# Kernel optimization log

Hardware: AMD Instinct MI355X
Metric: run time of the kernel (lower is better)

## Reference

```python
import jax, jax.numpy as jnp
from jax import lax
import numpy as np

H = 256

def _cell(x, h, c, wih, whh, bih, bhh):
    # PyTorch LSTMCell: gates ordered i, f, g, o
    g = x @ wih.T + bih + h @ whh.T + bhh
    i, f, gg, o = jnp.split(g, 4, axis=-1)
    c = jax.nn.sigmoid(f) * c + jax.nn.sigmoid(i) * jnp.tanh(gg)
    h = jax.nn.sigmoid(o) * jnp.tanh(c)
    return h, c


def setup_inputs() -> dict:
    key = jax.random.key(0)
    ks = iter(jax.random.split(key, 64))
    def lin(out_f, in_f):
        s = 1.0 / np.sqrt(in_f)
        w = jax.random.uniform(next(ks), (out_f, in_f), minval=-s, maxval=s, dtype=jnp.float32)
        b = jax.random.uniform(next(ks), (out_f,), minval=-s, maxval=s, dtype=jnp.float32)
        return w, b
    def cellp():
        s = 1.0 / np.sqrt(H)
        return tuple(jax.random.uniform(next(ks), sh, minval=-s, maxval=s, dtype=jnp.float32)
                     for sh in [(4 * H, H), (4 * H, H), (4 * H,), (4 * H,)])
    d = {}
    d['x'] = jax.random.normal(next(ks), (20, 256, 64, 64), dtype=jnp.float32)
    d['fc_en1_w'], d['fc_en1_b'] = lin(1024, 4096)
    d['fc_en2_w'], d['fc_en2_b'] = lin(H, 1024)
    for nm in ['en1', 'en2', 'en3', 'de1', 'de2', 'de3']:
        d[nm + '_wih'], d[nm + '_whh'], d[nm + '_bih'], d[nm + '_bhh'] = cellp()
    d['fc_de1_w'], d['fc_de1_b'] = lin(1024, H)
    d['fc_de2_w'], d['fc_de2_b'] = lin(4096, 1024)
    d['future_step'] = 10
    return d


def reference(x, fc_en1_w, fc_en1_b, fc_en2_w, fc_en2_b,
              en1_wih, en1_whh, en1_bih, en1_bhh,
              en2_wih, en2_whh, en2_bih, en2_bhh,
              en3_wih, en3_whh, en3_bih, en3_bhh,
              de1_wih, de1_whh, de1_bih, de1_bhh,
              de2_wih, de2_whh, de2_bih, de2_bhh,
              de3_wih, de3_whh, de3_bih, de3_bhh,
              fc_de1_w, fc_de1_b, fc_de2_w, fc_de2_b, future_step):
    seq, B = x.shape[0], x.shape[1]
    xf = x.reshape(seq, B, -1)  # (S, B, 4096)
    z0 = jnp.zeros((B, H), x.dtype)

    def enc_step(carry, xt):
        h1, c1, h2, c2, h3, c3 = carry
        z = jax.nn.relu(xt @ fc_en1_w.T + fc_en1_b)
        z = jax.nn.relu(z @ fc_en2_w.T + fc_en2_b)
        h1, c1 = _cell(z, h1, c1, en1_wih, en1_whh, en1_bih, en1_bhh)
        h2, c2 = _cell(h1, h2, c2, en2_wih, en2_whh, en2_bih, en2_bhh)
        h3, c3 = _cell(h2, h3, c3, en3_wih, en3_whh, en3_bih, en3_bhh)
        return (h1, c1, h2, c2, h3, c3), None

    enc_carry, _ = lax.scan(enc_step, (z0,) * 6, xf)
    h_e3 = enc_carry[4]

    def dec_step(carry, _):
        h1, c1, h2, c2, h3, c3 = carry
        h1, c1 = _cell(z0, h1, c1, de1_wih, de1_whh, de1_bih, de1_bhh)
        h2, c2 = _cell(h1, h2, c2, de2_wih, de2_whh, de2_bih, de2_bhh)
        h3, c3 = _cell(h2, h3, c3, de3_wih, de3_whh, de3_bih, de3_bhh)
        y = jax.nn.relu(h3 @ fc_de1_w.T + fc_de1_b)
        y = jnp.tanh(y @ fc_de2_w.T + fc_de2_b)
        return (h1, c1, h2, c2, h3, c3), y

    _, ys = lax.scan(dec_step, (h_e3, z0, z0, z0, z0, z0), None, length=future_step)
    return ys.reshape(future_step, B, 64, 64)
```

## Files before the change

### kernel.cpp

```cpp
#include <hip/hip_runtime.h>
#include <math.h>

static __device__ __forceinline__ float sigf(float v) { return 1.0f / (1.0f + expf(-v)); }

using s8v = __attribute__((ext_vector_type(8))) short;
using f4v = __attribute__((ext_vector_type(4))) float;

static __device__ __forceinline__ void splitf(float f, unsigned short& h, unsigned short& l) {
  unsigned u = __float_as_uint(f);
  unsigned short hb = (unsigned short)((u + 0x7FFFu + ((u >> 16) & 1u)) >> 16);
  float hf = __uint_as_float(((unsigned)hb) << 16);
  float lf = f - hf;
  unsigned ul = __float_as_uint(lf);
  unsigned short lb = (unsigned short)((ul + 0x7FFFu + ((ul >> 16) & 1u)) >> 16);
  h = hb; l = lb;
}

__global__ __launch_bounds__(256) void wsplit(
    const float* __restrict__ W, unsigned short* __restrict__ WH,
    unsigned short* __restrict__ WL, int n4)
{
  int i = blockIdx.x * 256 + threadIdx.x;
  if (i < n4) {
    float4 v = ((const float4*)W)[i];
    ushort4 h, l;
    splitf(v.x, h.x, l.x); splitf(v.y, h.y, l.y);
    splitf(v.z, h.z, l.z); splitf(v.w, h.w, l.w);
    ((ushort4*)WH)[i] = h;
    ((ushort4*)WL)[i] = l;
  }
}

template <int OSPLIT>
__global__ __launch_bounds__(256) void gemm_sf(
    const float* __restrict__ A,
    const unsigned short* __restrict__ WH, const unsigned short* __restrict__ WL,
    const float* __restrict__ bias, float* __restrict__ C,
    unsigned short* __restrict__ OH, unsigned short* __restrict__ OL,
    int M, int N, int K, int act)
{
  __shared__ unsigned short AsH[128 * 40];
  __shared__ unsigned short AsL[128 * 40];
  __shared__ unsigned short WsH[64 * 40];
  __shared__ unsigned short WsL[64 * 40];

  const int t = threadIdx.x;
  const int w = t >> 6, lane = t & 63;
  const int lrow = lane & 15, lk = (lane >> 4) * 8;
  const int m0 = blockIdx.x * 128, n0 = blockIdx.y * 64;

  f4v acc[2][4];
#pragma unroll
  for (int i = 0; i < 2; ++i)
#pragma unroll
    for (int j = 0; j < 4; ++j) acc[i][j] = (f4v){0.f, 0.f, 0.f, 0.f};

  for (int k0 = 0; k0 < K; k0 += 32) {
#pragma unroll
    for (int i = 0; i < 4; ++i) {
      int v = i * 256 + t;
      int row = v >> 3, kq = (v & 7) << 2;
      float4 a = *(const float4*)(A + (size_t)(m0 + row) * K + k0 + kq);
      ushort4 h4, l4;
      splitf(a.x, h4.x, l4.x); splitf(a.y, h4.y, l4.y);
      splitf(a.z, h4.z, l4.z); splitf(a.w, h4.w, l4.w);
      *(ushort4*)&AsH[row * 40 + kq] = h4;
      *(ushort4*)&AsL[row * 40 + kq] = l4;
    }
    {
      int row = t >> 2, q = (t & 3) * 8;
      *(s8v*)&WsH[row * 40 + q] = *(const s8v*)(WH + (size_t)(n0 + row) * K + k0 + q);
      *(s8v*)&WsL[row * 40 + q] = *(const s8v*)(WL + (size_t)(n0 + row) * K + k0 + q);
    }
    __syncthreads();

    s8v aH[2], aL[2], bH[4], bL[4];
#pragma unroll
    for (int mt = 0; mt < 2; ++mt) {
      int r = (w * 32 + mt * 16 + lrow) * 40 + lk;
      aH[mt] = *(const s8v*)&AsH[r];
      aL[mt] = *(const s8v*)&AsL[r];
    }
#pragma unroll
    for (int nt = 0; nt < 4; ++nt) {
      int r = (nt * 16 + lrow) * 40 + lk;
      bH[nt] = *(const s8v*)&WsH[r];
      bL[nt] = *(const s8v*)&WsL[r];
    }
#pragma unroll
    for (int mt = 0; mt < 2; ++mt)
#pragma unroll
      for (int nt = 0; nt < 4; ++nt) {
        acc[mt][nt] = __builtin_amdgcn_mfma_f32_16x16x32_bf16(aH[mt], bH[nt], acc[mt][nt], 0, 0, 0);
        acc[mt][nt] = __builtin_amdgcn_mfma_f32_16x16x32_bf16(aH[mt], bL[nt], acc[mt][nt], 0, 0, 0);
        acc[mt][nt] = __builtin_amdgcn_mfma_f32_16x16x32_bf16(aL[mt], bH[nt], acc[mt][nt], 0, 0, 0);
      }
    __syncthreads();
  }

#pragma unroll
  for (int mt = 0; mt < 2; ++mt)
#pragma unroll
    for (int nt = 0; nt < 4; ++nt) {
      int gcol = n0 + nt * 16 + lrow;
      float bv = bias[gcol];
#pragma unroll
      for (int r = 0; r < 4; ++r) {
        int grow = m0 + w * 32 + mt * 16 + (lane >> 4) * 4 + r;
        float v = acc[mt][nt][r] + bv;
        if (act == 1) v = fmaxf(v, 0.f);
        else if (act == 2) v = tanhf(v);
        if (OSPLIT) {
          unsigned short h, l;
          splitf(v, h, l);
          OH[(size_t)grow * N + gcol] = h;
          OL[(size_t)grow * N + gcol] = l;
        } else {
          C[(size_t)grow * N + gcol] = v;
        }
      }
    }
}

template <int OSPLIT>
__global__ __launch_bounds__(256) void gemm_bb(
    const unsigned short* __restrict__ AH, const unsigned short* __restrict__ AL,
    const unsigned short* __restrict__ WH, const unsigned short* __restrict__ WL,
    const float* __restrict__ bias, float* __restrict__ C,
    unsigned short* __restrict__ OH, unsigned short* __restrict__ OL,
    int M, int N, int K, int act)
{
  __shared__ unsigned short AsH[128 * 40];
  __shared__ unsigned short AsL[128 * 40];
  __shared__ unsigned short WsH[64 * 40];
  __shared__ unsigned short WsL[64 * 40];

  const int t = threadIdx.x;
  const int w = t >> 6, lane = t & 63;
  const int lrow = lane & 15, lk = (lane >> 4) * 8;
  const int m0 = blockIdx.x * 128, n0 = blockIdx.y * 64;

  f4v acc[2][4];
#pragma unroll
  for (int i = 0; i < 2; ++i)
#pragma unroll
    for (int j = 0; j < 4; ++j) acc[i][j] = (f4v){0.f, 0.f, 0.f, 0.f};

  for (int k0 = 0; k0 < K; k0 += 32) {
#pragma unroll
    for (int i = 0; i < 2; ++i) {
      int v = i * 256 + t;
      int row = v >> 2, q = (v & 3) * 8;
      *(s8v*)&AsH[row * 40 + q] = *(const s8v*)(AH + (size_t)(m0 + row) * K + k0 + q);
      *(s8v*)&AsL[row * 40 + q] = *(const s8v*)(AL + (size_t)(m0 + row) * K + k0 + q);
    }
    {
      int row = t >> 2, q = (t & 3) * 8;
      *(s8v*)&WsH[row * 40 + q] = *(const s8v*)(WH + (size_t)(n0 + row) * K + k0 + q);
      *(s8v*)&WsL[row * 40 + q] = *(const s8v*)(WL + (size_t)(n0 + row) * K + k0 + q);
    }
    __syncthreads();

    s8v aH[2], aL[2], bH[4], bL[4];
#pragma unroll
    for (int mt = 0; mt < 2; ++mt) {
      int r = (w * 32 + mt * 16 + lrow) * 40 + lk;
      aH[mt] = *(const s8v*)&AsH[r];
      aL[mt] = *(const s8v*)&AsL[r];
    }
#pragma unroll
    for (int nt = 0; nt < 4; ++nt) {
      int r = (nt * 16 + lrow) * 40 + lk;
      bH[nt] = *(const s8v*)&WsH[r];
      bL[nt] = *(const s8v*)&WsL[r];
    }
#pragma unroll
    for (int mt = 0; mt < 2; ++mt)
#pragma unroll
      for (int nt = 0; nt < 4; ++nt) {
        acc[mt][nt] = __builtin_amdgcn_mfma_f32_16x16x32_bf16(aH[mt], bH[nt], acc[mt][nt], 0, 0, 0);
        acc[mt][nt] = __builtin_amdgcn_mfma_f32_16x16x32_bf16(aH[mt], bL[nt], acc[mt][nt], 0, 0, 0);
        acc[mt][nt] = __builtin_amdgcn_mfma_f32_16x16x32_bf16(aL[mt], bH[nt], acc[mt][nt], 0, 0, 0);
      }
    __syncthreads();
  }

#pragma unroll
  for (int mt = 0; mt < 2; ++mt)
#pragma unroll
    for (int nt = 0; nt < 4; ++nt) {
      int gcol = n0 + nt * 16 + lrow;
      float bv = bias[gcol];
#pragma unroll
      for (int r = 0; r < 4; ++r) {
        int grow = m0 + w * 32 + mt * 16 + (lane >> 4) * 4 + r;
        float v = acc[mt][nt][r] + bv;
        if (act == 1) v = fmaxf(v, 0.f);
        else if (act == 2) v = tanhf(v);
        if (OSPLIT) {
          unsigned short h, l;
          splitf(v, h, l);
          OH[(size_t)grow * N + gcol] = h;
          OL[(size_t)grow * N + gcol] = l;
        } else {
          C[(size_t)grow * N + gcol] = v;
        }
      }
    }
}

__global__ __launch_bounds__(256) void prep_pack(
    const float* __restrict__ wih, const float* __restrict__ whh,
    const float* __restrict__ bih, const float* __restrict__ bhh,
    float* __restrict__ wihP, float* __restrict__ whhP, float* __restrict__ bP)
{
  const int j = blockIdx.x, k = threadIdx.x;
  float4 a, c;
  a.x = wih[(0 * 256 + j) * 256 + k];
  a.y = wih[(1 * 256 + j) * 256 + k];
  a.z = wih[(2 * 256 + j) * 256 + k];
  a.w = wih[(3 * 256 + j) * 256 + k];
  *(float4*)&wihP[((size_t)j * 256 + k) * 4] = a;
  c.x = whh[(0 * 256 + j) * 256 + k];
  c.y = whh[(1 * 256 + j) * 256 + k];
  c.z = whh[(2 * 256 + j) * 256 + k];
  c.w = whh[(3 * 256 + j) * 256 + k];
  *(float4*)&whhP[((size_t)j * 256 + k) * 4] = c;
  if (k < 4) bP[j * 4 + k] = bih[k * 256 + j] + bhh[k * 256 + j];
}

__global__ __launch_bounds__(256) void transpose256(
    const float* __restrict__ in, float* __restrict__ out)
{
  const int t = blockIdx.x, c4 = blockIdx.y;
  const int r = threadIdx.x;
  float4 v = *(const float4*)(in + ((size_t)t * 256 + r) * 256 + c4 * 4);
  float* op = out + (size_t)t * 65536 + (size_t)(c4 * 4) * 256 + r;
  op[0]   = v.x;
  op[256] = v.y;
  op[512] = v.z;
  op[768] = v.w;
}

__global__ __launch_bounds__(256) void transpose256s(
    const float* __restrict__ in, unsigned short* __restrict__ outH,
    unsigned short* __restrict__ outL)
{
  const int t = blockIdx.x, c4 = blockIdx.y;
  const int r = threadIdx.x;
  float4 v = *(const float4*)(in + ((size_t)t * 256 + r) * 256 + c4 * 4);
  ushort4 h, l;
  splitf(v.x, h.x, l.x); splitf(v.y, h.y, l.y);
  splitf(v.z, h.z, l.z); splitf(v.w, h.w, l.w);
  size_t o = (size_t)t * 65536 + (size_t)(c4 * 4) * 256 + r;
  outH[o] = h.x; outH[o + 256] = h.y; outH[o + 512] = h.z; outH[o + 768] = h.w;
  outL[o] = l.x; outL[o + 256] = l.y; outL[o + 512] = l.z; outL[o + 768] = l.w;
}

struct CellSlot {
  const float* x;
  const float* wih;
  const float* whh;
  const float* bias;
  const float* hin;
  float* c;
  float* hout;
  float* hcopy;
  int hasx;
};
struct CellArgs { CellSlot s[3]; };

__global__ __launch_bounds__(512) void cell_multi(CellArgs args)
{
  __shared__ float part[4][64][4];
  const CellSlot S = args.s[blockIdx.x >> 8];
  const int inner = blockIdx.x & 255;
  const int jg = inner & 63, bg = inner >> 6;
  const int t = threadIdx.x;
  const int lane = t & 63;
  const int wave = t >> 6;
  const int jwv = wave & 3;
  const int kh = __builtin_amdgcn_readfirstlane(wave >> 2);
  const int b = bg * 64 + lane;

  const int jw = __builtin_amdgcn_readfirstlane(jg * 4 + jwv);
  const float4* wh = (const float4*)(S.whh + (size_t)jw * 1024) + kh * 128;
  const float4* wi = (const float4*)(S.wih + (size_t)jw * 1024) + kh * 128;
  const float* hcol = S.hin + (size_t)kh * 128 * 256 + b;

  float4 acc;
  if (kh == 0) acc = *(const float4*)(S.bias + jw * 4);
  else         acc = (float4){0.f, 0.f, 0.f, 0.f};

  if (S.hasx) {
    const float* xcol = S.x + (size_t)kh * 128 * 256 + b;
#pragma unroll 8
    for (int k = 0; k < 128; ++k) {
      const float hv = hcol[k * 256];
      const float4 wv = wh[k];
      acc.x = fmaf(hv, wv.x, acc.x);
      acc.y = fmaf(hv, wv.y, acc.y);
      acc.z = fmaf(hv, wv.z, acc.z);
      acc.w = fmaf(hv, wv.w, acc.w);
      const float xv = xcol[k * 256];
      const float4 vv = wi[k];
      acc.x = fmaf(xv, vv.x, acc.x);
      acc.y = fmaf(xv, vv.y, acc.y);
      acc.z = fmaf(xv, vv.z, acc.z);
      acc.w = fmaf(xv, vv.w, acc.w);
    }
  } else {
#pragma unroll 8
    for (int k = 0; k < 128; ++k) {
      const float hv = hcol[k * 256];
      const float4 wv = wh[k];
      acc.x = fmaf(hv, wv.x, acc.x);
      acc.y = fmaf(hv, wv.y, acc.y);
      acc.z = fmaf(hv, wv.z, acc.z);
      acc.w = fmaf(hv, wv.w, acc.w);
    }
  }

  if (kh == 1) *(float4*)&part[jwv][lane][0] = acc;
  __syncthreads();
  if (kh == 0) {
    const float4 p = *(const float4*)&part[jwv][lane][0];
    acc.x += p.x; acc.y += p.y; acc.z += p.z; acc.w += p.w;

    const int idx = jw * 256 + b;
    const float cold = S.c[idx];
    const float ig = sigf(acc.x), fg = sigf(acc.y);
    const float gg = tanhf(acc.z), og = sigf(acc.w);
    const float cn = fg * cold + ig * gg;
    const float hn = og * tanhf(cn);
    S.c[idx] = cn;
    S.hout[idx] = hn;
    if (S.hcopy) S.hcopy[idx] = hn;
  }
}


extern "C" void kernel_launch(void* const* d_in, const int* in_sizes, int n_in,
                              void* d_out, int out_size, void* d_ws, size_t ws_size,
                              hipStream_t stream)
{
  const float* x_in  = (const float*)d_in[0];
  const float* w_en1 = (const float*)d_in[1];
  const float* b_en1 = (const float*)d_in[2];
  const float* w_en2 = (const float*)d_in[3];
  const float* b_en2 = (const float*)d_in[4];
  const float* cw[6][4];
  for (int i = 0; i < 6; ++i)
    for (int j = 0; j < 4; ++j) cw[i][j] = (const float*)d_in[5 + i * 4 + j];
  const float* w_de1 = (const float*)d_in[29];
  const float* b_de1 = (const float*)d_in[30];
  const float* w_de2 = (const float*)d_in[31];
  const float* b_de2 = (const float*)d_in[32];
  float* out = (float*)d_out;

  float* fs   = (float*)d_ws;
  float* wihP = fs;
  float* whhP = wihP + 6 * 262144;
  float* bP   = whhP + 6 * 262144;
  float* hb   = bP + 6 * 1024;
  float* cb   = hb + 12 * 65536;
  float* H3T  = cb + 6 * 65536;
  float* z2   = H3T + 10 * 65536;
  float* z2T  = z2 + 1310720;
  unsigned short* us = (unsigned short*)(z2T + 1310720);
  unsigned short* WEN1H = us;              us += 4194304;
  unsigned short* WEN1L = us;              us += 4194304;
  unsigned short* WEN2H = us;              us += 262144;
  unsigned short* WEN2L = us;              us += 262144;
  unsigned short* WDE1H = us;              us += 262144;
  unsigned short* WDE1L = us;              us += 262144;
  unsigned short* WDE2H = us;              us += 4194304;
  unsigned short* WDE2L = us;              us += 4194304;
  unsigned short* Z1H   = us;              us += 5242880;
  unsigned short* Z1L   = us;              us += 5242880;
  unsigned short* H3H = Z1H;
  unsigned short* H3L = Z1H + 655360;
  unsigned short* Y1H = Z1H + 1310720;
  unsigned short* Y1L = Z1H + 1310720 + 2621440;

  for (int i = 0; i < 6; ++i)
    prep_pack<<<256, 256, 0, stream>>>(cw[i][0], cw[i][1], cw[i][2], cw[i][3],
                                       wihP + i * 262144, whhP + i * 262144,
                                       bP + i * 1024);
  wsplit<<<4096, 256, 0, stream>>>(w_en1, WEN1H, WEN1L, 1048576);
  wsplit<<<256, 256, 0, stream>>>(w_en2, WEN2H, WEN2L, 65536);
  wsplit<<<256, 256, 0, stream>>>(w_de1, WDE1H, WDE1L, 65536);
  wsplit<<<4096, 256, 0, stream>>>(w_de2, WDE2H, WDE2L, 1048576);
  hipMemsetAsync(hb, 0, (size_t)18 * 65536 * sizeof(float), stream);

  gemm_sf<1><<<dim3(40, 16), 256, 0, stream>>>(
      x_in, WEN1H, WEN1L, b_en1, nullptr, Z1H, Z1L, 5120, 1024, 4096, 1);
  gemm_bb<0><<<dim3(40, 4), 256, 0, stream>>>(
      Z1H, Z1L, WEN2H, WEN2L, b_en2, z2, nullptr, nullptr, 5120, 256, 1024, 1);
  transpose256<<<dim3(20, 64), 256, 0, stream>>>(z2, z2T);

  int pp[6] = {0, 0, 0, 0, 0, 0};
  auto HBuf = [&](int l, int p) { return hb + (size_t)(l * 2 + p) * 65536; };
  auto CBuf = [&](int l) { return cb + (size_t)l * 65536; };
  auto WI = [&](int l) { return wihP + (size_t)l * 262144; };
  auto WHp = [&](int l) { return whhP + (size_t)l * 262144; };
  auto BB = [&](int l) { return bP + (size_t)l * 1024; };

  for (int s = 0; s <= 21; ++s) {
    CellArgs a; int n = 0; int tog[3]; int nt = 0;
    if (s < 20) {
      a.s[n++] = {z2T + (size_t)s * 65536, WI(0), WHp(0), BB(0),
                  HBuf(0, pp[0]), CBuf(0), HBuf(0, pp[0] ^ 1), nullptr, 1};
      tog[nt++] = 0;
    }
    if (s >= 1 && s <= 20) {
      a.s[n++] = {HBuf(0, pp[0]), WI(1), WHp(1), BB(1),
                  HBuf(1, pp[1]), CBuf(1), HBuf(1, pp[1] ^ 1), nullptr, 1};
      tog[nt++] = 1;
    }
    if (s >= 2) {
      a.s[n++] = {HBuf(1, pp[1]), WI(2), WHp(2), BB(2),
                  HBuf(2, pp[2]), CBuf(2), HBuf(2, pp[2] ^ 1), nullptr, 1};
      tog[nt++] = 2;
    }
    cell_multi<<<n * 256, 512, 0, stream>>>(a);
    for (int i = 0; i < nt; ++i) pp[tog[i]] ^= 1;
  }

  for (int s = 0; s <= 11; ++s) {
    CellArgs a; int n = 0; int tog[3]; int nt = 0;
    if (s < 10) {
      const float* h1in = (s == 0) ? HBuf(2, pp[2]) : HBuf(3, pp[3]);
      a.s[n++] = {nullptr, WI(3), WHp(3), BB(3),
                  h1in, CBuf(3), HBuf(3, pp[3] ^ 1), nullptr, 0};
      tog[nt++] = 3;
    }
    if (s >= 1 && s <= 10) {
      a.s[n++] = {HBuf(3, pp[3]), WI(4), WHp(4), BB(4),
                  HBuf(4, pp[4]), CBuf(4), HBuf(4, pp[4] ^ 1), nullptr, 1};
      tog[nt++] = 4;
    }
    if (s >= 2) {
      a.s[n++] = {HBuf(4, pp[4]), WI(5), WHp(5), BB(5),
                  HBuf(5, pp[5]), CBuf(5), HBuf(5, pp[5] ^ 1),
                  H3T + (size_t)(s - 2) * 65536, 1};
      tog[nt++] = 5;
    }
    cell_multi<<<n * 256, 512, 0, stream>>>(a);
    for (int i = 0; i < nt; ++i) pp[tog[i]] ^= 1;
  }

  transpose256s<<<dim3(10, 64), 256, 0, stream>>>(H3T, H3H, H3L);
  gemm_bb<1><<<dim3(20, 16), 256, 0, stream>>>(
      H3H, H3L, WDE1H, WDE1L, b_de1, nullptr, Y1H, Y1L, 2560, 1024, 256, 1);
  gemm_bb<0><<<dim3(20, 64), 256, 0, stream>>>(
      Y1H, Y1L, WDE2H, WDE2L, b_de2, out, nullptr, nullptr, 2560, 4096, 1024, 2);

  (void)in_sizes; (void)n_in; (void)out_size; (void)ws_size;
}
```

Measured before the change: 874.9 us.

## Split LSTM cell reduction four ways and pre-split input for bf16x3 GEMM

The LSTM cell kernel now uses 1024 threads per block, splitting the K reduction into four 64-wide quarters instead of two halves. Partial sums are combined through shared memory, which shortens each thread's serial FMA chain in the latency-bound recurrent steps at the cost of more waves per block and extra reductions. Separately, when the workspace is large enough, the input x is pre-split into bf16 high/low halves and the first encoder GEMM uses the bf16-pair kernel instead of the float-input split-on-the-fly kernel. This adds a large extra pass over the 20M-element input and 80MB of workspace.

Result: slower. 903.2 us (+3.2%).

```diff
diff --git a/kernel.cpp b/kernel.cpp
--- a/kernel.cpp
+++ b/kernel.cpp
@@ -270,9 +270,9 @@
 };
 struct CellArgs { CellSlot s[3]; };
 
-__global__ __launch_bounds__(512) void cell_multi(CellArgs args)
-{
-  __shared__ float part[4][64][4];
+__global__ __launch_bounds__(1024) void cell_multi(CellArgs args)
+{
+  __shared__ float part[3][4][64][4];
   const CellSlot S = args.s[blockIdx.x >> 8];
   const int inner = blockIdx.x & 255;
   const int jg = inner & 63, bg = inner >> 6;
@@ -280,22 +280,22 @@
   const int lane = t & 63;
   const int wave = t >> 6;
   const int jwv = wave & 3;
-  const int kh = __builtin_amdgcn_readfirstlane(wave >> 2);
+  const int kq = __builtin_amdgcn_readfirstlane(wave >> 2);
   const int b = bg * 64 + lane;
 
   const int jw = __builtin_amdgcn_readfirstlane(jg * 4 + jwv);
-  const float4* wh = (const float4*)(S.whh + (size_t)jw * 1024) + kh * 128;
-  const float4* wi = (const float4*)(S.wih + (size_t)jw * 1024) + kh * 128;
-  const float* hcol = S.hin + (size_t)kh * 128 * 256 + b;
+  const float4* wh = (const float4*)(S.whh + (size_t)jw * 1024) + kq * 64;
+  const float4* wi = (const float4*)(S.wih + (size_t)jw * 1024) + kq * 64;
+  const float* hcol = S.hin + (size_t)kq * 64 * 256 + b;
 
   float4 acc;
-  if (kh == 0) acc = *(const float4*)(S.bias + jw * 4);
+  if (kq == 0) acc = *(const float4*)(S.bias + jw * 4);
   else         acc = (float4){0.f, 0.f, 0.f, 0.f};
 
   if (S.hasx) {
-    const float* xcol = S.x + (size_t)kh * 128 * 256 + b;
+    const float* xcol = S.x + (size_t)kq * 64 * 256 + b;
 #pragma unroll 8
-    for (int k = 0; k < 128; ++k) {
+    for (int k = 0; k < 64; ++k) {
       const float hv = hcol[k * 256];
       const float4 wv = wh[k];
       acc.x = fmaf(hv, wv.x, acc.x);
@@ -311,7 +311,7 @@
     }
   } else {
 #pragma unroll 8
-    for (int k = 0; k < 128; ++k) {
+    for (int k = 0; k < 64; ++k) {
       const float hv = hcol[k * 256];
       const float4 wv = wh[k];
       acc.x = fmaf(hv, wv.x, acc.x);
@@ -321,11 +321,16 @@
     }
   }
 
-  if (kh == 1) *(float4*)&part[jwv][lane][0] = acc;
+  if (kq >= 1) *(float4*)&part[kq - 1][jwv][lane][0] = acc;
   __syncthreads();
-  if (kh == 0) {
-    const float4 p = *(const float4*)&part[jwv][lane][0];
-    acc.x += p.x; acc.y += p.y; acc.z += p.z; acc.w += p.w;
+  if (kq == 0) {
+    const float4 p0 = *(const float4*)&part[0][jwv][lane][0];
+    const float4 p1 = *(const float4*)&part[1][jwv][lane][0];
+    const float4 p2 = *(const float4*)&part[2][jwv][lane][0];
+    acc.x += p0.x + p1.x + p2.x;
+    acc.y += p0.y + p1.y + p2.y;
+    acc.z += p0.z + p1.z + p2.z;
+    acc.w += p0.w + p1.w + p2.w;
 
     const int idx = jw * 256 + b;
     const float cold = S.c[idx];
@@ -378,6 +383,10 @@
   unsigned short* WDE2L = us;              us += 4194304;
   unsigned short* Z1H   = us;              us += 5242880;
   unsigned short* Z1L   = us;              us += 5242880;
+  unsigned short* XH    = us;              us += 20971520;
+  unsigned short* XL    = us;              us += 20971520;
+  const size_t need_big = (size_t)((char*)us - (char*)d_ws);
+  const bool big = ws_size >= need_big;
   unsigned short* H3H = Z1H;
   unsigned short* H3L = Z1H + 655360;
   unsigned short* Y1H = Z1H + 1310720;
@@ -391,10 +400,16 @@
   wsplit<<<256, 256, 0, stream>>>(w_en2, WEN2H, WEN2L, 65536);
   wsplit<<<256, 256, 0, stream>>>(w_de1, WDE1H, WDE1L, 65536);
   wsplit<<<4096, 256, 0, stream>>>(w_de2, WDE2H, WDE2L, 1048576);
+  if (big)
+    wsplit<<<20480, 256, 0, stream>>>(x_in, XH, XL, 5242880);
   hipMemsetAsync(hb, 0, (size_t)18 * 65536 * sizeof(float), stream);
 
-  gemm_sf<1><<<dim3(40, 16), 256, 0, stream>>>(
-      x_in, WEN1H, WEN1L, b_en1, nullptr, Z1H, Z1L, 5120, 1024, 4096, 1);
+  if (big)
+    gemm_bb<1><<<dim3(40, 16), 256, 0, stream>>>(
+        XH, XL, WEN1H, WEN1L, b_en1, nullptr, Z1H, Z1L, 5120, 1024, 4096, 1);
+  else
+    gemm_sf<1><<<dim3(40, 16), 256, 0, stream>>>(
+        x_in, WEN1H, WEN1L, b_en1, nullptr, Z1H, Z1L, 5120, 1024, 4096, 1);
   gemm_bb<0><<<dim3(40, 4), 256, 0, stream>>>(
       Z1H, Z1L, WEN2H, WEN2L, b_en2, z2, nullptr, nullptr, 5120, 256, 1024, 1);
   transpose256<<<dim3(20, 64), 256, 0, stream>>>(z2, z2T);
@@ -423,7 +438,7 @@
                   HBuf(2, pp[2]), CBuf(2), HBuf(2, pp[2] ^ 1), nullptr, 1};
       tog[nt++] = 2;
     }
-    cell_multi<<<n * 256, 512, 0, stream>>>(a);
+    cell_multi<<<n * 256, 1024, 0, stream>>>(a);
     for (int i = 0; i < nt; ++i) pp[tog[i]] ^= 1;
   }
 
@@ -446,7 +461,7 @@
                   H3T + (size_t)(s - 2) * 65536, 1};
       tog[nt++] = 5;
     }
-    cell_multi<<<n * 256, 512, 0, stream>>>(a);
+    cell_multi<<<n * 256, 1024, 0, stream>>>(a);
     for (int i = 0; i < nt; ++i) pp[tog[i]] ^= 1;
   }
 
```
